# Performance work log

Measured on AMD Instinct MI355X. Metric: run time of the kernel, lower is better.

The kernel has to match this reference:

```python
import jax, jax.numpy as jnp
import numpy as np

B, F, BOND, NFREQ, NOUT, INIT_STD = 16384, 256, 16, 4, 1, 0.1


def setup_inputs() -> dict:
    key = jax.random.key(0)
    ks = jax.random.split(key, 10)
    x = jax.random.uniform(ks[0], (B, F), dtype=jnp.float32)
    inp = {"x": x, "frequency_min": jnp.array(1.0, dtype=jnp.float32)}
    d_in = 1 + 2 * NFREQ  # physical leg dim = 9
    n, level = F, 0
    while n > 1:
        n2 = n // 2
        d_out = NOUT if n == 2 else BOND
        # stack all same-level node tensors: [n_pairs, d_left, d_right, d_out]
        inp[f"W{level}"] = jax.random.normal(ks[level + 1], (n2, d_in, d_in, d_out), dtype=jnp.float32) * INIT_STD
        d_in, n, level = d_out, n2, level + 1
    return inp


def reference(x, frequency_min, W0, W1, W2, W3, W4, W5, W6, W7):
    Ws = [W0, W1, W2, W3, W4, W5, W6, W7]
    nfreq = (W0.shape[1] - 1) // 2
    # Fourier feature map: [B, F, 1+2*nfreq]
    xs = (x * frequency_min)[..., None]
    freqs = jnp.arange(1, nfreq + 1, dtype=x.dtype)
    feats = jnp.concatenate(
        [jnp.ones_like(xs), jnp.sin(xs * freqs), jnp.cos(xs * freqs)], axis=-1
    )
    nodes = feats  # [B, n_nodes, d]
    for W in Ws:
        left = nodes[:, 0::2]   # [B, n/2, d]
        right = nodes[:, 1::2]  # [B, n/2, d]
        # batched pairwise bilinear contraction over all nodes of one level
        nodes = jnp.einsum('bni,nijd,bnj->bnd', left, W, right)
    return nodes[:, 0, :]  # [B, NOUT]
```

## Files before the change

kernel.cpp:

```cpp
#include <hip/hip_runtime.h>
#include <math.h>

#define BTOT 16384

typedef __attribute__((ext_vector_type(8))) short s16x8;
typedef __attribute__((ext_vector_type(4))) float f32x4;
typedef __attribute__((ext_vector_type(4))) uint u32x4;
typedef __attribute__((ext_vector_type(2))) float f32x2;
typedef __attribute__((ext_vector_type(2))) uint u32x2;

#define OFF0 0u
#define OFF1 655360u
#define OFF2 1179648u
#define OFF3 1441792u
#define OFF4 1572864u
#define OFF5 1638400u
#define OFF6 1671168u
#define OFF7 1687552u

__device__ __forceinline__ ushort rtn_bf16(float x) {
  uint u = __builtin_bit_cast(uint, x);
  uint r = u + 0x7fffu + ((u >> 16) & 1u);
  return (ushort)(r >> 16);
}

__global__ __launch_bounds__(256) void wprep_kernel(
    const float* __restrict__ W0, const float* __restrict__ W1,
    const float* __restrict__ W2, const float* __restrict__ W3,
    const float* __restrict__ W4, const float* __restrict__ W5,
    const float* __restrict__ W6, const float* __restrict__ W7,
    ushort* __restrict__ U) {
  int blk = blockIdx.x;
  const float* Wsrc; ushort* dst; int ktN, din; bool dout1 = false;
  if (blk < 128)      { Wsrc = W0 + blk * 1296;         dst = U + OFF0 + (size_t)blk * 5120;         ktN = 5; din = 9;  }
  else if (blk < 192) { Wsrc = W1 + (blk - 128) * 4096; dst = U + OFF1 + (size_t)(blk - 128) * 8192; ktN = 8; din = 16; }
  else if (blk < 224) { Wsrc = W2 + (blk - 192) * 4096; dst = U + OFF2 + (size_t)(blk - 192) * 8192; ktN = 8; din = 16; }
  else if (blk < 240) { Wsrc = W3 + (blk - 224) * 4096; dst = U + OFF3 + (size_t)(blk - 224) * 8192; ktN = 8; din = 16; }
  else if (blk < 248) { Wsrc = W4 + (blk - 240) * 4096; dst = U + OFF4 + (size_t)(blk - 240) * 8192; ktN = 8; din = 16; }
  else if (blk < 252) { Wsrc = W5 + (blk - 248) * 4096; dst = U + OFF5 + (size_t)(blk - 248) * 8192; ktN = 8; din = 16; }
  else if (blk < 254) { Wsrc = W6 + (blk - 252) * 4096; dst = U + OFF6 + (size_t)(blk - 252) * 8192; ktN = 8; din = 16; }
  else                { Wsrc = W7;                      dst = U + OFF7;                              ktN = 8; din = 16; dout1 = true; }
  int entries = ktN * 512;
  for (int e = threadIdx.x; e < entries; e += 256) {
    int kt = e >> 9, l = (e >> 3) & 63, jv = e & 7;
    int k = kt * 32 + ((l >> 4) << 3) + jv;
    int i = k >> 4, j = k & 15, n = l & 15;
    float w;
    if (dout1) w = (n == 0) ? Wsrc[i * 16 + j] : 0.f;
    else       w = (i < din && j < din) ? Wsrc[(i * din + j) * 16 + n] : 0.f;
    uint u = __builtin_bit_cast(uint, w);
    uint h = u & 0xffff0000u;
    dst[e] = (ushort)(h >> 16);
    dst[entries + e] = rtn_bf16(w - __builtin_bit_cast(float, h));
  }
}

template <int KTN, bool L0M>
__device__ __forceinline__ f32x4 mfma_core(const float* Lcol, const float* Rcol,
                                           const int ld, const ushort* __restrict__ Wf,
                                           int lane) {
  const int g = lane >> 4;
  const int j0 = (g & 1) * 8, gh = g >> 1;
  const float* Lg = Lcol + gh * ld;
  float lf[KTN];
#pragma unroll
  for (int i = 0; i < KTN; ++i) lf[i] = Lg[2 * i * ld];
  f32x2 rf2[4];
#pragma unroll
  for (int j = 0; j < 8; ++j) {
    float v = (L0M && (j0 + j >= 9)) ? 0.f : Rcol[(j0 + j) * ld];
    rf2[j >> 1][j & 1] = v;
  }
  f32x4 acc = {0.f, 0.f, 0.f, 0.f};
  const int entries = KTN * 512;
#pragma unroll
  for (int kt = 0; kt < KTN; ++kt) {
    const s16x8 wh = *(const s16x8*)&Wf[(kt * 64 + lane) * 8];
    const s16x8 wl = *(const s16x8*)&Wf[entries + (kt * 64 + lane) * 8];
    const f32x2 li2 = {lf[kt], lf[kt]};
    u32x4 hv, lv;
#pragma unroll
    for (int jp = 0; jp < 4; ++jp) {
      f32x2 p2 = li2 * rf2[jp];
      u32x2 u2 = __builtin_bit_cast(u32x2, p2);
      u32x2 hb = u2 & 0xffff0000u;
      f32x2 h2 = __builtin_bit_cast(f32x2, hb);
      f32x2 q2 = __builtin_elementwise_fma(li2, rf2[jp], -h2);
      u32x2 uq = __builtin_bit_cast(u32x2, q2);
      hv[jp] = __builtin_amdgcn_perm(u2.y, u2.x, 0x07060302u);
      lv[jp] = __builtin_amdgcn_perm(uq.y, uq.x, 0x07060302u);
    }
    s16x8 ahi = __builtin_bit_cast(s16x8, hv);
    s16x8 alo = __builtin_bit_cast(s16x8, lv);
    acc = __builtin_amdgcn_mfma_f32_16x16x32_bf16(ahi, wh, acc, 0, 0, 0);
    acc = __builtin_amdgcn_mfma_f32_16x16x32_bf16(alo, wh, acc, 0, 0, 0);
    acc = __builtin_amdgcn_mfma_f32_16x16x32_bf16(ahi, wl, acc, 0, 0, 0);
  }
  return acc;
}

#define LDF 67

__device__ __forceinline__ void feats_col(float xv, float* Fb, int col) {
  float s1 = __sinf(xv), c1 = __cosf(xv);
  Fb[0 * LDF + col] = 1.f; Fb[1 * LDF + col] = s1; Fb[5 * LDF + col] = c1;
  float sk = s1, ck = c1;
#pragma unroll
  for (int k = 2; k <= 4; ++k) {
    float sn = s1 * ck + c1 * sk, cn = c1 * ck - s1 * sk;
    sk = sn; ck = cn;
    Fb[k * LDF + col] = sk; Fb[(4 + k) * LDF + col] = ck;
  }
}

__global__ __launch_bounds__(256, 4) void ttn_front_kernel(
    const float* __restrict__ x, const float* __restrict__ fminp,
    const ushort* __restrict__ U, float* __restrict__ s1out) {
  __shared__ float F0[10 * LDF], F1[10 * LDF];
  __shared__ float A0[16 * LDF], B0[16 * LDF];
  __shared__ float A1[16 * LDF], B1[16 * LDF];
  __shared__ float A2[16 * LDF], B2[16 * LDF];

  const int tid = threadIdx.x;
  const int lane = tid & 63, w = tid >> 6;
  const int m = lane & 15, g = lane >> 4;
  const int bl = w * 16 + m;
  const int b0 = blockIdx.x * 64;
  const int s = blockIdx.y;
  const float fmin = fminp[0];

  if (lane < 32) {
    int col = w * 16 + (lane & 15);
    ((lane >> 4) ? F1 : F0)[9 * LDF + col] = 0.f;
  }

  const float* xw = x + (size_t)(b0 + w * 16 + (lane & 15)) * 256 + s * 16;
  float* outG = s1out + (size_t)(s * 16) * BTOT + b0;

  auto storeL = [&](f32x4 a, float* Out) {
#pragma unroll
    for (int r = 0; r < 4; ++r) Out[m * LDF + w * 16 + g * 4 + r] = a[r];
  };

  for (int t = 0; t < 8; ++t) {
    if (lane < 32) {
      int side = lane >> 4;
      float xv = xw[2 * t + side] * fmin;
      feats_col(xv, side ? F1 : F0, w * 16 + (lane & 15));
    }
    f32x4 a = mfma_core<5, true>(&F0[bl], &F1[bl], LDF,
                                 U + OFF0 + (size_t)(8 * s + t) * 5120, lane);
    storeL(a, (t & 1) ? B0 : A0);
    if (t & 1) {
      f32x4 c1 = mfma_core<8, false>(&A0[bl], &B0[bl], LDF,
                                     U + OFF1 + (size_t)(4 * s + (t >> 1)) * 8192, lane);
      storeL(c1, ((t >> 1) & 1) ? B1 : A1);
      if ((t & 3) == 3) {
        f32x4 c2 = mfma_core<8, false>(&A1[bl], &B1[bl], LDF,
                                       U + OFF2 + (size_t)(2 * s + (t >> 2)) * 8192, lane);
        storeL(c2, ((t >> 2) & 1) ? B2 : A2);
        if (t == 7) {
          f32x4 c3 = mfma_core<8, false>(&A2[bl], &B2[bl], LDF,
                                         U + OFF3 + (size_t)s * 8192, lane);
#pragma unroll
          for (int r = 0; r < 4; ++r)
            outG[(size_t)m * BTOT + w * 16 + g * 4 + r] = c3[r];
        }
      }
    }
  }
}

__global__ __launch_bounds__(256) void ttn_back_kernel(
    const float* __restrict__ s1, const ushort* __restrict__ U,
    float* __restrict__ out) {
  __shared__ float T[256 * 17];
  const int tid = threadIdx.x;
  const int lane = tid & 63, w = tid >> 6;
  const int m = lane & 15, g = lane >> 4;
  const int b0 = blockIdx.x * 16;

#pragma unroll
  for (int it = 0; it < 4; ++it) {
    int idx = it * 256 + tid;
    int r = idx >> 2, c4 = (idx & 3) * 4;
    float4 v = *(const float4*)&s1[(size_t)r * BTOT + b0 + c4];
    T[r * 17 + c4 + 0] = v.x; T[r * 17 + c4 + 1] = v.y;
    T[r * 17 + c4 + 2] = v.z; T[r * 17 + c4 + 3] = v.w;
  }
  __syncthreads();

  const int q = w, base = 64 * q;
  f32x4 a0 = mfma_core<8, false>(&T[base * 17 + m], &T[(base + 16) * 17 + m], 17,
                                 U + OFF4 + (size_t)(2 * q) * 8192, lane);
  f32x4 a1 = mfma_core<8, false>(&T[(base + 32) * 17 + m], &T[(base + 48) * 17 + m], 17,
                                 U + OFF4 + (size_t)(2 * q + 1) * 8192, lane);
#pragma unroll
  for (int r = 0; r < 4; ++r) {
    T[(base + m) * 17 + g * 4 + r] = a0[r];
    T[(base + 32 + m) * 17 + g * 4 + r] = a1[r];
  }
  f32x4 a2 = mfma_core<8, false>(&T[base * 17 + m], &T[(base + 32) * 17 + m], 17,
                                 U + OFF5 + (size_t)q * 8192, lane);
#pragma unroll
  for (int r = 0; r < 4; ++r) T[(base + m) * 17 + g * 4 + r] = a2[r];
  __syncthreads();

  if (w < 2) {
    f32x4 a3 = mfma_core<8, false>(&T[(128 * w) * 17 + m], &T[(128 * w + 64) * 17 + m],
                                   17, U + OFF6 + (size_t)w * 8192, lane);
#pragma unroll
    for (int r = 0; r < 4; ++r) T[(128 * w + m) * 17 + g * 4 + r] = a3[r];
  }
  __syncthreads();

  if (w == 0) {
    f32x4 a4 = mfma_core<8, false>(&T[m], &T[128 * 17 + m], 17, U + OFF7, lane);
    if (m == 0) {
#pragma unroll
      for (int r = 0; r < 4; ++r) out[b0 + g * 4 + r] = a4[r];
    }
  }
}

extern "C" void kernel_launch(void* const* d_in, const int* in_sizes, int n_in,
                              void* d_out, int out_size, void* d_ws, size_t ws_size,
                              hipStream_t stream) {
  const float* x    = (const float*)d_in[0];
  const float* fmin = (const float*)d_in[1];
  const float* W0   = (const float*)d_in[2];
  const float* W1   = (const float*)d_in[3];
  const float* W2   = (const float*)d_in[4];
  const float* W3   = (const float*)d_in[5];
  const float* W4   = (const float*)d_in[6];
  const float* W5   = (const float*)d_in[7];
  const float* W6   = (const float*)d_in[8];
  const float* W7   = (const float*)d_in[9];
  float* out = (float*)d_out;

  ushort* U = (ushort*)d_ws;
  float* s1 = (float*)((char*)d_ws + (4u << 20));

  wprep_kernel<<<255, 256, 0, stream>>>(W0, W1, W2, W3, W4, W5, W6, W7, U);
  ttn_front_kernel<<<dim3(256, 16), 256, 0, stream>>>(x, fmin, U, s1);
  ttn_back_kernel<<<1024, 256, 0, stream>>>(s1, U, out);
}
```

Before: 237.1 us.

## Use single-wave blocks in front kernel, each wave handling two 16-sample tiles

Measured after the change: 237.3 us. About the same (+0.1%).

```diff
diff --git a/kernel.cpp b/kernel.cpp
--- a/kernel.cpp
+++ b/kernel.cpp
@@ -55,6 +55,29 @@
   }
 }
 
+__device__ __forceinline__ f32x4 split3(float li, const f32x2* rf2,
+                                        s16x8 wh, s16x8 wl, f32x4 acc) {
+  const f32x2 li2 = {li, li};
+  u32x4 hv, lv;
+#pragma unroll
+  for (int jp = 0; jp < 4; ++jp) {
+    f32x2 p2 = li2 * rf2[jp];
+    u32x2 u2 = __builtin_bit_cast(u32x2, p2);
+    u32x2 hb = u2 & 0xffff0000u;
+    f32x2 h2 = __builtin_bit_cast(f32x2, hb);
+    f32x2 q2 = __builtin_elementwise_fma(li2, rf2[jp], -h2);
+    u32x2 uq = __builtin_bit_cast(u32x2, q2);
+    hv[jp] = __builtin_amdgcn_perm(u2.y, u2.x, 0x07060302u);
+    lv[jp] = __builtin_amdgcn_perm(uq.y, uq.x, 0x07060302u);
+  }
+  s16x8 ahi = __builtin_bit_cast(s16x8, hv);
+  s16x8 alo = __builtin_bit_cast(s16x8, lv);
+  acc = __builtin_amdgcn_mfma_f32_16x16x32_bf16(ahi, wh, acc, 0, 0, 0);
+  acc = __builtin_amdgcn_mfma_f32_16x16x32_bf16(alo, wh, acc, 0, 0, 0);
+  acc = __builtin_amdgcn_mfma_f32_16x16x32_bf16(ahi, wl, acc, 0, 0, 0);
+  return acc;
+}
+
 template <int KTN, bool L0M>
 __device__ __forceinline__ f32x4 mfma_core(const float* Lcol, const float* Rcol,
                                            const int ld, const ushort* __restrict__ Wf,
@@ -77,94 +100,111 @@
   for (int kt = 0; kt < KTN; ++kt) {
     const s16x8 wh = *(const s16x8*)&Wf[(kt * 64 + lane) * 8];
     const s16x8 wl = *(const s16x8*)&Wf[entries + (kt * 64 + lane) * 8];
-    const f32x2 li2 = {lf[kt], lf[kt]};
-    u32x4 hv, lv;
-#pragma unroll
-    for (int jp = 0; jp < 4; ++jp) {
-      f32x2 p2 = li2 * rf2[jp];
-      u32x2 u2 = __builtin_bit_cast(u32x2, p2);
-      u32x2 hb = u2 & 0xffff0000u;
-      f32x2 h2 = __builtin_bit_cast(f32x2, hb);
-      f32x2 q2 = __builtin_elementwise_fma(li2, rf2[jp], -h2);
-      u32x2 uq = __builtin_bit_cast(u32x2, q2);
-      hv[jp] = __builtin_amdgcn_perm(u2.y, u2.x, 0x07060302u);
-      lv[jp] = __builtin_amdgcn_perm(uq.y, uq.x, 0x07060302u);
-    }
-    s16x8 ahi = __builtin_bit_cast(s16x8, hv);
-    s16x8 alo = __builtin_bit_cast(s16x8, lv);
-    acc = __builtin_amdgcn_mfma_f32_16x16x32_bf16(ahi, wh, acc, 0, 0, 0);
-    acc = __builtin_amdgcn_mfma_f32_16x16x32_bf16(alo, wh, acc, 0, 0, 0);
-    acc = __builtin_amdgcn_mfma_f32_16x16x32_bf16(ahi, wl, acc, 0, 0, 0);
+    acc = split3(lf[kt], rf2, wh, wl, acc);
   }
   return acc;
 }
 
-#define LDF 67
-
-__device__ __forceinline__ void feats_col(float xv, float* Fb, int col) {
+template <int KTN, bool L0M>
+__device__ __forceinline__ void mfma_core2(const float* Lb, const float* Rb,
+                                           const int ld, const ushort* __restrict__ Wf,
+                                           int lane, f32x4& o0, f32x4& o1) {
+  const int g = lane >> 4;
+  const int j0 = (g & 1) * 8, gh = g >> 1;
+  const float* Lg = Lb + gh * ld;
+  float lf0[KTN], lf1[KTN];
+#pragma unroll
+  for (int i = 0; i < KTN; ++i) {
+    lf0[i] = Lg[2 * i * ld];
+    lf1[i] = Lg[2 * i * ld + 16];
+  }
+  f32x2 rf0[4], rf1[4];
+#pragma unroll
+  for (int j = 0; j < 8; ++j) {
+    bool z = L0M && (j0 + j >= 9);
+    rf0[j >> 1][j & 1] = z ? 0.f : Rb[(j0 + j) * ld];
+    rf1[j >> 1][j & 1] = z ? 0.f : Rb[(j0 + j) * ld + 16];
+  }
+  f32x4 a0 = {0.f, 0.f, 0.f, 0.f}, a1 = {0.f, 0.f, 0.f, 0.f};
+  const int entries = KTN * 512;
+#pragma unroll
+  for (int kt = 0; kt < KTN; ++kt) {
+    const s16x8 wh = *(const s16x8*)&Wf[(kt * 64 + lane) * 8];
+    const s16x8 wl = *(const s16x8*)&Wf[entries + (kt * 64 + lane) * 8];
+    a0 = split3(lf0[kt], rf0, wh, wl, a0);
+    a1 = split3(lf1[kt], rf1, wh, wl, a1);
+  }
+  o0 = a0; o1 = a1;
+}
+
+#define LDW 35
+
+__device__ __forceinline__ void feats_col_ld(float xv, float* Fb, int col, int ld) {
   float s1 = __sinf(xv), c1 = __cosf(xv);
-  Fb[0 * LDF + col] = 1.f; Fb[1 * LDF + col] = s1; Fb[5 * LDF + col] = c1;
+  Fb[0 * ld + col] = 1.f; Fb[1 * ld + col] = s1; Fb[5 * ld + col] = c1;
   float sk = s1, ck = c1;
 #pragma unroll
   for (int k = 2; k <= 4; ++k) {
     float sn = s1 * ck + c1 * sk, cn = c1 * ck - s1 * sk;
     sk = sn; ck = cn;
-    Fb[k * LDF + col] = sk; Fb[(4 + k) * LDF + col] = ck;
-  }
-}
-
-__global__ __launch_bounds__(256, 4) void ttn_front_kernel(
+    Fb[k * ld + col] = sk; Fb[(4 + k) * ld + col] = ck;
+  }
+}
+
+__global__ __launch_bounds__(64, 2) void ttn_front_kernel(
     const float* __restrict__ x, const float* __restrict__ fminp,
     const ushort* __restrict__ U, float* __restrict__ s1out) {
-  __shared__ float F0[10 * LDF], F1[10 * LDF];
-  __shared__ float A0[16 * LDF], B0[16 * LDF];
-  __shared__ float A1[16 * LDF], B1[16 * LDF];
-  __shared__ float A2[16 * LDF], B2[16 * LDF];
-
-  const int tid = threadIdx.x;
-  const int lane = tid & 63, w = tid >> 6;
+  __shared__ float F0[10 * LDW], F1[10 * LDW];
+  __shared__ float A0[16 * LDW], B0[16 * LDW];
+  __shared__ float A1[16 * LDW], B1[16 * LDW];
+  __shared__ float A2[16 * LDW], B2[16 * LDW];
+
+  const int lane = threadIdx.x;
   const int m = lane & 15, g = lane >> 4;
-  const int bl = w * 16 + m;
-  const int b0 = blockIdx.x * 64;
+  const int b0 = blockIdx.x * 32;
   const int s = blockIdx.y;
   const float fmin = fminp[0];
 
-  if (lane < 32) {
-    int col = w * 16 + (lane & 15);
-    ((lane >> 4) ? F1 : F0)[9 * LDF + col] = 0.f;
-  }
-
-  const float* xw = x + (size_t)(b0 + w * 16 + (lane & 15)) * 256 + s * 16;
+  if (lane < 32) F0[9 * LDW + lane] = 0.f;
+  else           F1[9 * LDW + (lane - 32)] = 0.f;
+
+  const int xc = lane & 31, xside = lane >> 5;
+  const float* xw = x + (size_t)(b0 + xc) * 256 + s * 16 + xside;
   float* outG = s1out + (size_t)(s * 16) * BTOT + b0;
 
-  auto storeL = [&](f32x4 a, float* Out) {
-#pragma unroll
-    for (int r = 0; r < 4; ++r) Out[m * LDF + w * 16 + g * 4 + r] = a[r];
+  auto storeL2 = [&](f32x4 a0s, f32x4 a1s, float* Out) {
+#pragma unroll
+    for (int r = 0; r < 4; ++r) {
+      Out[m * LDW + g * 4 + r] = a0s[r];
+      Out[m * LDW + 16 + g * 4 + r] = a1s[r];
+    }
   };
 
   for (int t = 0; t < 8; ++t) {
-    if (lane < 32) {
-      int side = lane >> 4;
-      float xv = xw[2 * t + side] * fmin;
-      feats_col(xv, side ? F1 : F0, w * 16 + (lane & 15));
-    }
-    f32x4 a = mfma_core<5, true>(&F0[bl], &F1[bl], LDF,
-                                 U + OFF0 + (size_t)(8 * s + t) * 5120, lane);
-    storeL(a, (t & 1) ? B0 : A0);
+    feats_col_ld(xw[2 * t] * fmin, xside ? F1 : F0, xc, LDW);
+    f32x4 a0, a1;
+    mfma_core2<5, true>(&F0[m], &F1[m], LDW,
+                        U + OFF0 + (size_t)(8 * s + t) * 5120, lane, a0, a1);
+    storeL2(a0, a1, (t & 1) ? B0 : A0);
     if (t & 1) {
-      f32x4 c1 = mfma_core<8, false>(&A0[bl], &B0[bl], LDF,
-                                     U + OFF1 + (size_t)(4 * s + (t >> 1)) * 8192, lane);
-      storeL(c1, ((t >> 1) & 1) ? B1 : A1);
+      f32x4 c0, c1;
+      mfma_core2<8, false>(&A0[m], &B0[m], LDW,
+                           U + OFF1 + (size_t)(4 * s + (t >> 1)) * 8192, lane, c0, c1);
+      storeL2(c0, c1, ((t >> 1) & 1) ? B1 : A1);
       if ((t & 3) == 3) {
-        f32x4 c2 = mfma_core<8, false>(&A1[bl], &B1[bl], LDF,
-                                       U + OFF2 + (size_t)(2 * s + (t >> 2)) * 8192, lane);
-        storeL(c2, ((t >> 2) & 1) ? B2 : A2);
+        f32x4 d0, d1;
+        mfma_core2<8, false>(&A1[m], &B1[m], LDW,
+                             U + OFF2 + (size_t)(2 * s + (t >> 2)) * 8192, lane, d0, d1);
+        storeL2(d0, d1, ((t >> 2) & 1) ? B2 : A2);
         if (t == 7) {
-          f32x4 c3 = mfma_core<8, false>(&A2[bl], &B2[bl], LDF,
-                                         U + OFF3 + (size_t)s * 8192, lane);
-#pragma unroll
-          for (int r = 0; r < 4; ++r)
-            outG[(size_t)m * BTOT + w * 16 + g * 4 + r] = c3[r];
+          f32x4 e0, e1;
+          mfma_core2<8, false>(&A2[m], &B2[m], LDW,
+                               U + OFF3 + (size_t)s * 8192, lane, e0, e1);
+#pragma unroll
+          for (int r = 0; r < 4; ++r) {
+            outG[(size_t)m * BTOT + g * 4 + r] = e0[r];
+            outG[(size_t)m * BTOT + 16 + g * 4 + r] = e1[r];
+          }
         }
       }
     }
@@ -242,6 +282,6 @@
   float* s1 = (float*)((char*)d_ws + (4u << 20));
 
   wprep_kernel<<<255, 256, 0, stream>>>(W0, W1, W2, W3, W4, W5, W6, W7, U);
-  ttn_front_kernel<<<dim3(256, 16), 256, 0, stream>>>(x, fmin, U, s1);
+  ttn_front_kernel<<<dim3(BTOT / 32, 16), 64, 0, stream>>>(x, fmin, U, s1);
   ttn_back_kernel<<<1024, 256, 0, stream>>>(s1, U, out);
 }
```

## Restructure back kernel to read level-4 inputs from global directly with fewer waves

Applied to the files above, without the earlier changes.

After: 238.6 us. No clear change (+0.6%).

```diff
diff --git a/kernel.cpp b/kernel.cpp
--- a/kernel.cpp
+++ b/kernel.cpp
@@ -55,6 +55,29 @@
   }
 }
 
+__device__ __forceinline__ f32x4 split3(float li, const f32x2* rf2,
+                                        s16x8 wh, s16x8 wl, f32x4 acc) {
+  const f32x2 li2 = {li, li};
+  u32x4 hv, lv;
+#pragma unroll
+  for (int jp = 0; jp < 4; ++jp) {
+    f32x2 p2 = li2 * rf2[jp];
+    u32x2 u2 = __builtin_bit_cast(u32x2, p2);
+    u32x2 hb = u2 & 0xffff0000u;
+    f32x2 h2 = __builtin_bit_cast(f32x2, hb);
+    f32x2 q2 = __builtin_elementwise_fma(li2, rf2[jp], -h2);
+    u32x2 uq = __builtin_bit_cast(u32x2, q2);
+    hv[jp] = __builtin_amdgcn_perm(u2.y, u2.x, 0x07060302u);
+    lv[jp] = __builtin_amdgcn_perm(uq.y, uq.x, 0x07060302u);
+  }
+  s16x8 ahi = __builtin_bit_cast(s16x8, hv);
+  s16x8 alo = __builtin_bit_cast(s16x8, lv);
+  acc = __builtin_amdgcn_mfma_f32_16x16x32_bf16(ahi, wh, acc, 0, 0, 0);
+  acc = __builtin_amdgcn_mfma_f32_16x16x32_bf16(alo, wh, acc, 0, 0, 0);
+  acc = __builtin_amdgcn_mfma_f32_16x16x32_bf16(ahi, wl, acc, 0, 0, 0);
+  return acc;
+}
+
 template <int KTN, bool L0M>
 __device__ __forceinline__ f32x4 mfma_core(const float* Lcol, const float* Rcol,
                                            const int ld, const ushort* __restrict__ Wf,
@@ -77,24 +100,7 @@
   for (int kt = 0; kt < KTN; ++kt) {
     const s16x8 wh = *(const s16x8*)&Wf[(kt * 64 + lane) * 8];
     const s16x8 wl = *(const s16x8*)&Wf[entries + (kt * 64 + lane) * 8];
-    const f32x2 li2 = {lf[kt], lf[kt]};
-    u32x4 hv, lv;
-#pragma unroll
-    for (int jp = 0; jp < 4; ++jp) {
-      f32x2 p2 = li2 * rf2[jp];
-      u32x2 u2 = __builtin_bit_cast(u32x2, p2);
-      u32x2 hb = u2 & 0xffff0000u;
-      f32x2 h2 = __builtin_bit_cast(f32x2, hb);
-      f32x2 q2 = __builtin_elementwise_fma(li2, rf2[jp], -h2);
-      u32x2 uq = __builtin_bit_cast(u32x2, q2);
-      hv[jp] = __builtin_amdgcn_perm(u2.y, u2.x, 0x07060302u);
-      lv[jp] = __builtin_amdgcn_perm(uq.y, uq.x, 0x07060302u);
-    }
-    s16x8 ahi = __builtin_bit_cast(s16x8, hv);
-    s16x8 alo = __builtin_bit_cast(s16x8, lv);
-    acc = __builtin_amdgcn_mfma_f32_16x16x32_bf16(ahi, wh, acc, 0, 0, 0);
-    acc = __builtin_amdgcn_mfma_f32_16x16x32_bf16(alo, wh, acc, 0, 0, 0);
-    acc = __builtin_amdgcn_mfma_f32_16x16x32_bf16(ahi, wl, acc, 0, 0, 0);
+    acc = split3(lf[kt], rf2, wh, wl, acc);
   }
   return acc;
 }
@@ -171,54 +177,50 @@
   }
 }
 
-__global__ __launch_bounds__(256) void ttn_back_kernel(
+__global__ __launch_bounds__(128) void ttn_back_kernel(
     const float* __restrict__ s1, const ushort* __restrict__ U,
     float* __restrict__ out) {
-  __shared__ float T[256 * 17];
+  __shared__ float P[2][2][16 * 17];
+  __shared__ float S[4][16 * 17];
   const int tid = threadIdx.x;
   const int lane = tid & 63, w = tid >> 6;
   const int m = lane & 15, g = lane >> 4;
   const int b0 = blockIdx.x * 16;
 
-#pragma unroll
-  for (int it = 0; it < 4; ++it) {
-    int idx = it * 256 + tid;
-    int r = idx >> 2, c4 = (idx & 3) * 4;
-    float4 v = *(const float4*)&s1[(size_t)r * BTOT + b0 + c4];
-    T[r * 17 + c4 + 0] = v.x; T[r * 17 + c4 + 1] = v.y;
-    T[r * 17 + c4 + 2] = v.z; T[r * 17 + c4 + 3] = v.w;
+  auto storeC = [&](f32x4 a, float* Buf) {
+#pragma unroll
+    for (int r = 0; r < 4; ++r) Buf[m * 17 + g * 4 + r] = a[r];
+  };
+
+#pragma unroll
+  for (int h = 0; h < 2; ++h) {
+    const int n0 = 4 * w + 2 * h;
+#pragma unroll
+    for (int p = 0; p < 2; ++p) {
+      const int n = n0 + p;
+      f32x4 a = mfma_core<8, false>(&s1[(size_t)(32 * n) * BTOT + b0 + m],
+                                    &s1[(size_t)(32 * n + 16) * BTOT + b0 + m],
+                                    BTOT, U + OFF4 + (size_t)n * 8192, lane);
+      storeC(a, P[w][p]);
+    }
+    f32x4 a5 = mfma_core<8, false>(&P[w][0][m], &P[w][1][m], 17,
+                                   U + OFF5 + (size_t)(2 * w + h) * 8192, lane);
+    storeC(a5, S[2 * w + h]);
   }
   __syncthreads();
 
-  const int q = w, base = 64 * q;
-  f32x4 a0 = mfma_core<8, false>(&T[base * 17 + m], &T[(base + 16) * 17 + m], 17,
-                                 U + OFF4 + (size_t)(2 * q) * 8192, lane);
-  f32x4 a1 = mfma_core<8, false>(&T[(base + 32) * 17 + m], &T[(base + 48) * 17 + m], 17,
-                                 U + OFF4 + (size_t)(2 * q + 1) * 8192, lane);
-#pragma unroll
-  for (int r = 0; r < 4; ++r) {
-    T[(base + m) * 17 + g * 4 + r] = a0[r];
-    T[(base + 32 + m) * 17 + g * 4 + r] = a1[r];
-  }
-  f32x4 a2 = mfma_core<8, false>(&T[base * 17 + m], &T[(base + 32) * 17 + m], 17,
-                                 U + OFF5 + (size_t)q * 8192, lane);
-#pragma unroll
-  for (int r = 0; r < 4; ++r) T[(base + m) * 17 + g * 4 + r] = a2[r];
+  {
+    f32x4 a6 = mfma_core<8, false>(&S[2 * w][m], &S[2 * w + 1][m], 17,
+                                   U + OFF6 + (size_t)w * 8192, lane);
+    storeC(a6, S[2 * w]);
+  }
   __syncthreads();
 
-  if (w < 2) {
-    f32x4 a3 = mfma_core<8, false>(&T[(128 * w) * 17 + m], &T[(128 * w + 64) * 17 + m],
-                                   17, U + OFF6 + (size_t)w * 8192, lane);
-#pragma unroll
-    for (int r = 0; r < 4; ++r) T[(128 * w + m) * 17 + g * 4 + r] = a3[r];
-  }
-  __syncthreads();
-
   if (w == 0) {
-    f32x4 a4 = mfma_core<8, false>(&T[m], &T[128 * 17 + m], 17, U + OFF7, lane);
+    f32x4 a7 = mfma_core<8, false>(&S[0][m], &S[2][m], 17, U + OFF7, lane);
     if (m == 0) {
 #pragma unroll
-      for (int r = 0; r < 4; ++r) out[b0 + g * 4 + r] = a4[r];
+      for (int r = 0; r < 4; ++r) out[b0 + g * 4 + r] = a7[r];
     }
   }
 }
@@ -243,5 +245,5 @@
 
   wprep_kernel<<<255, 256, 0, stream>>>(W0, W1, W2, W3, W4, W5, W6, W7, U);
   ttn_front_kernel<<<dim3(256, 16), 256, 0, stream>>>(x, fmin, U, s1);
-  ttn_back_kernel<<<1024, 256, 0, stream>>>(s1, U, out);
-}
+  ttn_back_kernel<<<1024, 128, 0, stream>>>(s1, U, out);
+}
```
